# Kernel tuning notes

Hardware: AMD Instinct MI355X
Metric: run time of the kernel (lower is better)

The kernel has to match this reference:

```python
import jax, jax.numpy as jnp
import numpy as np

BN_EPS = 1e-5


def setup_inputs() -> dict:
    key = jax.random.key(0)
    ks = jax.random.split(key, 6)
    B, C, N = 8, 256, 4096
    C4 = C // 4
    return {
        "x": jax.random.normal(ks[0], (B, C, N), dtype=jnp.float32),
        "w_qk": jax.random.normal(ks[1], (C4, C), dtype=jnp.float32) * 0.05,  # shared q/k weight
        "w_v": jax.random.normal(ks[2], (C, C), dtype=jnp.float32) * 0.05,
        "b_v": jax.random.normal(ks[3], (C,), dtype=jnp.float32) * 0.05,
        "w_t": jax.random.normal(ks[4], (C, C), dtype=jnp.float32) * 0.05,
        "b_t": jax.random.normal(ks[5], (C,), dtype=jnp.float32) * 0.05,
        "gamma": jnp.ones((C,), dtype=jnp.float32),
        "beta": jnp.zeros((C,), dtype=jnp.float32),
        "run_mean": jnp.zeros((C,), dtype=jnp.float32),
        "run_var": jnp.ones((C,), dtype=jnp.float32),
    }


def reference(x, w_qk, w_v, b_v, w_t, b_t, gamma, beta, run_mean, run_var):
    # x: [B, C, N]; 1x1 Conv1d == channel matmul.
    x_q = jnp.einsum('oc,bcn->bno', w_qk, x)               # [B, N, C/4]
    x_k = jnp.einsum('oc,bcn->bon', w_qk, x)               # [B, C/4, N]
    energy = jnp.einsum('bno,bom->bnm', x_q, x_k)          # [B, N, N], NO 1/sqrt(d) scaling
    attn = jax.nn.softmax(energy, axis=-1)                 # softmax over last dim only
    x_v = jnp.einsum('oc,bcn->bon', w_v, x) + b_v[None, :, None]  # [B, C, N]
    x_r = jnp.einsum('bcn,bnm->bcm', x_v, attn)            # V @ attn (right-multiply, no transpose)
    t = jnp.einsum('oc,bcn->bon', w_t, x - x_r) + b_t[None, :, None]
    # BatchNorm1d (inference): per-channel affine with running stats
    inv = gamma / jnp.sqrt(run_var + BN_EPS)
    bn = t * inv[None, :, None] + (beta - run_mean * inv)[None, :, None]
    return x + jnp.maximum(bn, 0.0)
```

## Files before the change

### kernel.cpp

```cpp
#include <hip/hip_runtime.h>

#define Bb 8
#define Cc 256
#define C4 64
#define Nn 4096

typedef _Float16 half8 __attribute__((ext_vector_type(8)));
typedef float f32x4 __attribute__((ext_vector_type(4)));
typedef unsigned int u32;

__device__ __forceinline__ f32x4 fz4() {
  f32x4 z; z[0] = 0.f; z[1] = 0.f; z[2] = 0.f; z[3] = 0.f; return z;
}
__device__ __forceinline__ f32x4 mfma16(half8 a, half8 b, f32x4 c) {
  return __builtin_amdgcn_mfma_f32_16x16x32_f16(a, b, c, 0, 0, 0);
}
__device__ __forceinline__ u32 pkrtz(float a, float b) {
  typedef __fp16 h2n __attribute__((ext_vector_type(2)));
  h2n h = __builtin_amdgcn_cvt_pkrtz(a, b);
  return __builtin_bit_cast(u32, h);
}
__device__ __forceinline__ float ex2(float x) {
  float r;
  asm("v_exp_f32 %0, %1" : "=v"(r) : "v"(x));
  return r;
}
__device__ __forceinline__ void gll16(const void* g, void* l) {
  __builtin_amdgcn_global_load_lds(
      (const __attribute__((address_space(1))) u32*)g,
      (__attribute__((address_space(3))) u32*)l, 16, 0, 0);
}


__global__ void k0_weights(const float* __restrict__ wqk, const float* __restrict__ wv,
                           const float* __restrict__ wt,
                           _Float16* __restrict__ wqkh, _Float16* __restrict__ wqkl,
                           _Float16* __restrict__ wvf, _Float16* __restrict__ wtf) {
  int idx = blockIdx.x * 256 + threadIdx.x;
  if (idx < C4 * Cc) {
    int o = idx >> 8, c = idx & 255;
    float f = wqk[idx] * 1.2011224087864498f;
    _Float16 h = (_Float16)f;
    int off = ((((o >> 4) * 8 + (c >> 5)) * 4 + ((c >> 3) & 3)) * 16 + (o & 15)) * 8 + (c & 7);
    wqkh[off] = h;
    wqkl[off] = (_Float16)(f - (float)h);
  }
  if (idx < Cc * Cc) {
    int o = idx >> 8, k = idx & 255;
    int off = ((((o >> 4) * 8 + (k >> 5)) * 4 + ((k >> 3) & 3)) * 16 + (o & 15)) * 8 + (k & 7);
    wvf[off] = (_Float16)wv[idx];
    wtf[off] = (_Float16)wt[idx];
  }
}

__global__ __launch_bounds__(512) void k23_qkv(
    const float* __restrict__ x,
    const _Float16* __restrict__ wqkh, const _Float16* __restrict__ wqkl,
    const _Float16* __restrict__ wvf, const float* __restrict__ bv,
    _Float16* __restrict__ qkf, _Float16* __restrict__ xvf) {
  __shared__ _Float16 xh[64 * 264];
  const int bid = blockIdx.x;
  const int b = bid & 7, n0 = (bid >> 3) * 64, tid = threadIdx.x;
  {
    const int cc = tid >> 3, nn = (tid & 7) * 8;
    #pragma unroll
    for (int ph = 0; ph < 4; ++ph) {
      int c = cc + ph * 64;
      const float* src = x + ((size_t)(b * Cc + c)) * Nn + n0 + nn;
      float4 v0 = *(const float4*)(src);
      float4 v1 = *(const float4*)(src + 4);
      float vv[8] = {v0.x, v0.y, v0.z, v0.w, v1.x, v1.y, v1.z, v1.w};
      #pragma unroll
      for (int j = 0; j < 8; ++j) xh[(nn + j) * 264 + c] = (_Float16)vv[j];
    }
  }
  __syncthreads();
  const int w = tid >> 6, lane = tid & 63, l15 = lane & 15, l4 = lane >> 4;
  {
    const int fn = w >> 1, ob = (w & 1) * 32;
    f32x4 acc[2] = {fz4(), fz4()};
    #pragma unroll
    for (int kb = 0; kb < 8; ++kb) {
      half8 ah = *(const half8*)(xh + (fn * 16 + l15) * 264 + kb * 32 + l4 * 8);
      #pragma unroll
      for (int f = 0; f < 2; ++f) {
        const int ot = (ob >> 4) + f;
        half8 bh = *(const half8*)((const char*)wqkh + (ot * 8 + kb) * 1024 + lane * 16);
        half8 bl = *(const half8*)((const char*)wqkl + (ot * 8 + kb) * 1024 + lane * 16);
        acc[f] = mfma16(ah, bh, acc[f]);
        acc[f] = mfma16(ah, bl, acc[f]);
      }
    }
    #pragma unroll
    for (int f = 0; f < 2; ++f)
      #pragma unroll
      for (int i = 0; i < 4; ++i) {
        const int n = n0 + fn * 16 + l4 * 4 + i;
        const int o = ob + f * 16 + l15;
        int off = ((((b * 256 + (n >> 4)) * 2 + (o >> 5)) * 4 + ((o >> 3) & 3)) * 16 +
                   (n & 15)) * 8 + (o & 7);
        qkf[off] = (_Float16)acc[f][i];
      }
  }
  {
    const int cb = w * 32;
    f32x4 acc[2][4];
    #pragma unroll
    for (int a = 0; a < 2; ++a)
      #pragma unroll
      for (int q = 0; q < 4; ++q) acc[a][q] = fz4();
    #pragma unroll
    for (int kb = 0; kb < 8; ++kb) {
      half8 bfr[4];
      #pragma unroll
      for (int fnb = 0; fnb < 4; ++fnb)
        bfr[fnb] = *(const half8*)(xh + (fnb * 16 + l15) * 264 + kb * 32 + l4 * 8);
      #pragma unroll
      for (int fc = 0; fc < 2; ++fc) {
        const int ct = (cb >> 4) + fc;
        half8 a = *(const half8*)((const char*)wvf + (ct * 8 + kb) * 1024 + lane * 16);
        #pragma unroll
        for (int fnb = 0; fnb < 4; ++fnb)
          acc[fc][fnb] = mfma16(a, bfr[fnb], acc[fc][fnb]);
      }
    }
    #pragma unroll
    for (int fc = 0; fc < 2; ++fc)
      #pragma unroll
      for (int fnb = 0; fnb < 4; ++fnb)
        #pragma unroll
        for (int i = 0; i < 4; ++i) {
          const int c = cb + fc * 16 + l4 * 4 + i;
          const int n = n0 + fnb * 16 + l15;
          int off = ((((b * 16 + (c >> 4)) * 128 + (n >> 5)) * 4 + ((n >> 3) & 3)) * 16 +
                     (c & 15)) * 8 + (n & 7);
          xvf[off] = (_Float16)(acc[fc][fnb][i] + bv[c]);
        }
  }
}

__global__ __launch_bounds__(512, 4) void k4_stats(
    const _Float16* __restrict__ qkf, float* __restrict__ stats) {
  __shared__ float red[64][8];
  const int bid = blockIdx.x;
  const int b = bid & 7, n0 = (bid >> 3) * 64, tid = threadIdx.x;
  const int w = tid >> 6, lane = tid & 63, l15 = lane & 15, l4 = lane >> 4;
  const char* qbt = (const char*)qkf + (size_t)b * 524288;

  half8 qn_r[2][4];
  #pragma unroll
  for (int kb = 0; kb < 2; ++kb)
    #pragma unroll
    for (int fn = 0; fn < 4; ++fn)
      qn_r[kb][fn] = *(const half8*)(qbt + (((n0 >> 4) + fn) * 2 + kb) * 1024 + lane * 16);

  const char* qp = qbt + w * 2048 + lane * 16;
  half8 qa0 = *(const half8*)qp;
  half8 qa1 = *(const half8*)(qp + 1024);

  float sm[4] = {0.f, 0.f, 0.f, 0.f};
  for (int it = 0; it < 32; ++it) {
    f32x4 g[4] = {fz4(), fz4(), fz4(), fz4()};
    #pragma unroll
    for (int fn = 0; fn < 4; ++fn) g[fn] = mfma16(qa0, qn_r[0][fn], g[fn]);
    #pragma unroll
    for (int fn = 0; fn < 4; ++fn) g[fn] = mfma16(qa1, qn_r[1][fn], g[fn]);
    if (it < 31) qp += 16384;
    qa0 = *(const half8*)qp;
    qa1 = *(const half8*)(qp + 1024);
    #pragma unroll
    for (int fn = 0; fn < 4; ++fn)
      #pragma unroll
      for (int i = 0; i < 4; ++i)
        sm[fn] += ex2(g[fn][i] - 32.0f);
  }
  #pragma unroll
  for (int fn = 0; fn < 4; ++fn) {
    sm[fn] += __shfl_xor(sm[fn], 16, 64);
    sm[fn] += __shfl_xor(sm[fn], 32, 64);
  }
  if (l4 == 0) {
    #pragma unroll
    for (int fn = 0; fn < 4; ++fn) red[fn * 16 + l15][w] = sm[fn];
  }
  __syncthreads();
  if (tid < 64) {
    float t = 0.f;
    #pragma unroll
    for (int j = 0; j < 8; ++j) t += red[tid][j];
    stats[(size_t)b * Nn + n0 + tid] = 32.0f + log2f(t);
  }
}

__global__ __launch_bounds__(512, 2) void k5_main(
    const float* __restrict__ x,
    const _Float16* __restrict__ qkf, const _Float16* __restrict__ xvf,
    const float* __restrict__ stats,
    const _Float16* __restrict__ wtf, const float* __restrict__ bt,
    const float* __restrict__ gamma, const float* __restrict__ beta,
    const float* __restrict__ rmean, const float* __restrict__ rvar,
    float* __restrict__ out) {
  __shared__ __align__(16) char smem[122880];
  const int bid = blockIdx.x;
  const int b = bid & 7, m0 = (bid >> 3) * 128, tid = threadIdx.x;
  const int w = tid >> 6, lane = tid & 63, l15 = lane & 15, l4 = lane >> 4;
  const int wa = w >> 2;
  const int wb = w & 3;
  const size_t bq = (size_t)b * Nn;
  const char* qkt = (const char*)qkf + (size_t)b * 524288;
  const char* xvt = (const char*)xvf + (size_t)b * 2097152;
  const int key = l15 & 7;

  half8 qm_r[2][4];
  #pragma unroll
  for (int kb = 0; kb < 2; ++kb)
    #pragma unroll
    for (int fm = 0; fm < 4; ++fm)
      qm_r[kb][fm] = *(const half8*)(qkt + ((((m0 >> 4) + wa * 4 + fm) * 2) + kb) * 1024 +
                                     lane * 16);

  const char* qnsrc = qkt + 16384 + (size_t)tid * 16;
  const char* xvp = xvt + (size_t)w * 262144 + (size_t)lane * 16;
  const float* anp = stats + bq + wb * 16 + l4 * 4;

  f32x4 acc[4][4];
  #pragma unroll
  for (int a = 0; a < 4; ++a)
    #pragma unroll
    for (int q = 0; q < 4; ++q) acc[a][q] = fz4();

  gll16(qkt + (size_t)tid * 16, smem + w * 1024);
  gll16(qkt + 8192 + (size_t)tid * 16, smem + 8192 + w * 1024);
  #pragma unroll
  for (int j = 0; j < 4; ++j)
    gll16(xvp + (j >> 1) * 131072 + (j & 1) * 1024, smem + 57344 + (w * 4 + j) * 1024);
  float4 an = *(const float4*)anp;
  asm volatile("s_waitcnt vmcnt(0) lgkmcnt(0)" ::: "memory");
  __builtin_amdgcn_sched_barrier(0);
  __builtin_amdgcn_s_barrier();

  int br = 0, bw = 2;
  for (int it = 0; it < 64; ++it) {
    gll16(qnsrc, smem + bw * 8192 + w * 1024);
    if (it < 61) qnsrc += 8192;
    bw = bw == 2 ? 0 : bw + 1;
    const char* qb = smem + br * 8192;
    br = br == 2 ? 0 : br + 1;
    f32x4 g[4] = {fz4(), fz4(), fz4(), fz4()};
    #pragma unroll
    for (int kb = 0; kb < 2; ++kb) {
      half8 ah = *(const half8*)(qb + (wb * 2 + kb) * 1024 + lane * 16);
      #pragma unroll
      for (int fm = 0; fm < 4; ++fm)
        g[fm] = mfma16(ah, qm_r[kb][fm], g[fm]);
    }
    char* PTp = smem + 24576 + ((it & 1) << 14);
    #pragma unroll
    for (int fm = 0; fm < 4; ++fm) {
      uint2 pk;
      pk.x = pkrtz(ex2(g[fm][0] - an.x), ex2(g[fm][1] - an.y));
      pk.y = pkrtz(ex2(g[fm][2] - an.z), ex2(g[fm][3] - an.w));
      *(uint2*)(PTp + (wa * 64 + fm * 16 + l15) * 128 +
                ((wb * 32 + l4 * 8) ^ (key << 4))) = pk;
    }
    if (it < 63) anp += 64;
    an = *(const float4*)anp;
    asm volatile("s_waitcnt vmcnt(2) lgkmcnt(0)" ::: "memory");
    __builtin_amdgcn_sched_barrier(0);
    __builtin_amdgcn_s_barrier();
    const char* xvR = smem + 57344 + ((it & 1) << 15);
    __builtin_amdgcn_s_setprio(1);
    #pragma unroll
    for (int kb = 0; kb < 2; ++kb) {
      half8 pa[4], xb[4];
      #pragma unroll
      for (int fm = 0; fm < 4; ++fm)
        pa[fm] = *(const half8*)(PTp + (wa * 64 + fm * 16 + l15) * 128 +
                                 (((kb * 4 + l4) ^ key) * 16));
      #pragma unroll
      for (int fc = 0; fc < 4; ++fc)
        xb[fc] = *(const half8*)(xvR + ((wb * 4 + fc) * 2 + kb) * 1024 + lane * 16);
      #pragma unroll
      for (int fm = 0; fm < 4; ++fm)
        #pragma unroll
        for (int fc = 0; fc < 4; ++fc)
          acc[fm][fc] = mfma16(pa[fm], xb[fc], acc[fm][fc]);
    }
    __builtin_amdgcn_s_setprio(0);
    if (it < 63) xvp += 2048;
    char* xvD = smem + 57344 + (((it + 1) & 1) << 15) + (w * 4) * 1024;
    #pragma unroll
    for (int j = 0; j < 4; ++j)
      gll16(xvp + (j >> 1) * 131072 + (j & 1) * 1024, xvD + j * 1024);
  }
  asm volatile("s_waitcnt vmcnt(0) lgkmcnt(0)" ::: "memory");
  __builtin_amdgcn_sched_barrier(0);
  __builtin_amdgcn_s_barrier();

  _Float16* st = (_Float16*)smem;
  #pragma unroll
  for (int fm = 0; fm < 4; ++fm)
    #pragma unroll
    for (int fc = 0; fc < 4; ++fc) {
      int c = wb * 64 + fc * 16 + l15;
      int mb = wa * 64 + fm * 16 + l4 * 4;
      const float* xp = x + ((size_t)b * Cc + c) * Nn + m0 + mb;
      float4 v = *(const float4*)xp;
      float vv[4] = {v.x, v.y, v.z, v.w};
      #pragma unroll
      for (int i = 0; i < 4; ++i)
        st[(mb + i) * 264 + c] = (_Float16)(vv[i] - acc[fm][fc][i]);
    }
  __syncthreads();
  {
    const int ob = wb * 64, mh = wa * 64;
    f32x4 t[4][4];
    #pragma unroll
    for (int a = 0; a < 4; ++a)
      #pragma unroll
      for (int q = 0; q < 4; ++q) t[a][q] = fz4();
    #pragma unroll
    for (int kb = 0; kb < 8; ++kb) {
      half8 bfr[4];
      #pragma unroll
      for (int fm2 = 0; fm2 < 4; ++fm2)
        bfr[fm2] = *(const half8*)(st + (mh + fm2 * 16 + l15) * 264 + kb * 32 + l4 * 8);
      #pragma unroll
      for (int fo = 0; fo < 4; ++fo) {
        const int ot = (ob >> 4) + fo;
        half8 a = *(const half8*)((const char*)wtf + (ot * 8 + kb) * 1024 + lane * 16);
        #pragma unroll
        for (int fm2 = 0; fm2 < 4; ++fm2)
          t[fo][fm2] = mfma16(a, bfr[fm2], t[fo][fm2]);
      }
    }
    #pragma unroll
    for (int fo = 0; fo < 4; ++fo)
      #pragma unroll
      for (int i = 0; i < 4; ++i) {
        const int o = ob + fo * 16 + l4 * 4 + i;
        const float inv = gamma[o] * rsqrtf(rvar[o] + 1e-5f);
        const float addv = beta[o] - rmean[o] * inv;
        const float btv = bt[o];
        #pragma unroll
        for (int fm2 = 0; fm2 < 4; ++fm2) {
          const int m = m0 + mh + fm2 * 16 + l15;
          float tv = t[fo][fm2][i] + btv;
          float bn = tv * inv + addv;
          float xr = x[((size_t)b * Cc + o) * Nn + m];
          out[((size_t)b * Cc + o) * Nn + m] = xr + fmaxf(bn, 0.0f);
        }
      }
  }
}

extern "C" void kernel_launch(void* const* d_in, const int* in_sizes, int n_in,
                              void* d_out, int out_size, void* d_ws, size_t ws_size,
                              hipStream_t stream) {
  const float* x = (const float*)d_in[0];
  const float* wqk = (const float*)d_in[1];
  const float* wv = (const float*)d_in[2];
  const float* bv = (const float*)d_in[3];
  const float* wt = (const float*)d_in[4];
  const float* bt = (const float*)d_in[5];
  const float* gamma = (const float*)d_in[6];
  const float* beta = (const float*)d_in[7];
  const float* rmean = (const float*)d_in[8];
  const float* rvar = (const float*)d_in[9];
  float* out = (float*)d_out;

  char* ws = (char*)d_ws;
  size_t off = 0;
  auto alloc = [&](size_t nb) {
    char* p = ws + off;
    off += (nb + 255) & ~(size_t)255;
    return p;
  };
  _Float16* qkf = (_Float16*)alloc((size_t)Bb * Nn * C4 * 2);
  _Float16* xvf = (_Float16*)alloc((size_t)Bb * Cc * Nn * 2);
  float* stats = (float*)alloc((size_t)Bb * Nn * 4);
  _Float16* wqkh = (_Float16*)alloc((size_t)C4 * Cc * 2);
  _Float16* wqkl = (_Float16*)alloc((size_t)C4 * Cc * 2);
  _Float16* wvf = (_Float16*)alloc((size_t)Cc * Cc * 2);
  _Float16* wtf = (_Float16*)alloc((size_t)Cc * Cc * 2);

  k0_weights<<<dim3(256), dim3(256), 0, stream>>>(wqk, wv, wt, wqkh, wqkl, wvf, wtf);
  k23_qkv<<<dim3(512), dim3(512), 0, stream>>>(x, wqkh, wqkl, wvf, bv, qkf, xvf);
  k4_stats<<<dim3(512), dim3(512), 0, stream>>>(qkf, stats);
  k5_main<<<dim3(256), dim3(512), 0, stream>>>(x, qkf, xvf, stats, wtf, bt,
                                               gamma, beta, rmean, rvar, out);
}
```

Baseline: 149.2 us.

## Load Q/K and V tiles directly into registers instead of LDS staging

Drops the global_load_lds triple/double-buffered staging of the key tiles and V tiles in the main attention kernel. Each wave now prefetches its own fragments into ping-pong register sets one iteration ahead. The softmax row stats are preloaded once into LDS rather than fetched per iteration. LDS use falls from about 120 KB to 68 KB, which may allow two blocks per CU. The cost is duplicated global/L2 traffic across waves, higher register pressure, and a last-iteration prefetch that reads past the batch's slice.

```diff
diff --git a/kernel.cpp b/kernel.cpp
--- a/kernel.cpp
+++ b/kernel.cpp
@@ -24,11 +24,6 @@
   float r;
   asm("v_exp_f32 %0, %1" : "=v"(r) : "v"(x));
   return r;
-}
-__device__ __forceinline__ void gll16(const void* g, void* l) {
-  __builtin_amdgcn_global_load_lds(
-      (const __attribute__((address_space(1))) u32*)g,
-      (__attribute__((address_space(3))) u32*)l, 16, 0, 0);
 }
 
 
@@ -200,7 +195,7 @@
     const float* __restrict__ gamma, const float* __restrict__ beta,
     const float* __restrict__ rmean, const float* __restrict__ rvar,
     float* __restrict__ out) {
-  __shared__ __align__(16) char smem[122880];
+  __shared__ __align__(16) char smem[69632];
   const int bid = blockIdx.x;
   const int b = bid & 7, m0 = (bid >> 3) * 128, tid = threadIdx.x;
   const int w = tid >> 6, lane = tid & 63, l15 = lane & 15, l4 = lane >> 4;
@@ -210,6 +205,7 @@
   const char* qkt = (const char*)qkf + (size_t)b * 524288;
   const char* xvt = (const char*)xvf + (size_t)b * 2097152;
   const int key = l15 & 7;
+  float* anL = (float*)smem;
 
   half8 qm_r[2][4];
   #pragma unroll
@@ -219,9 +215,8 @@
       qm_r[kb][fm] = *(const half8*)(qkt + ((((m0 >> 4) + wa * 4 + fm) * 2) + kb) * 1024 +
                                      lane * 16);
 
-  const char* qnsrc = qkt + 16384 + (size_t)tid * 16;
-  const char* xvp = xvt + (size_t)w * 262144 + (size_t)lane * 16;
-  const float* anp = stats + bq + wb * 16 + l4 * 4;
+  const char* ah_base = qkt + (wb * 2) * 1024 + (size_t)lane * 16;
+  const char* xb_base = xvt + (size_t)(wb * 4) * 131072 + (size_t)lane * 16;
 
   f32x4 acc[4][4];
   #pragma unroll
@@ -229,71 +224,73 @@
     #pragma unroll
     for (int q = 0; q < 4; ++q) acc[a][q] = fz4();
 
-  gll16(qkt + (size_t)tid * 16, smem + w * 1024);
-  gll16(qkt + 8192 + (size_t)tid * 16, smem + 8192 + w * 1024);
-  #pragma unroll
-  for (int j = 0; j < 4; ++j)
-    gll16(xvp + (j >> 1) * 131072 + (j & 1) * 1024, smem + 57344 + (w * 4 + j) * 1024);
-  float4 an = *(const float4*)anp;
-  asm volatile("s_waitcnt vmcnt(0) lgkmcnt(0)" ::: "memory");
-  __builtin_amdgcn_sched_barrier(0);
-  __builtin_amdgcn_s_barrier();
-
-  int br = 0, bw = 2;
-  for (int it = 0; it < 64; ++it) {
-    gll16(qnsrc, smem + bw * 8192 + w * 1024);
-    if (it < 61) qnsrc += 8192;
-    bw = bw == 2 ? 0 : bw + 1;
-    const char* qb = smem + br * 8192;
-    br = br == 2 ? 0 : br + 1;
-    f32x4 g[4] = {fz4(), fz4(), fz4(), fz4()};
-    #pragma unroll
-    for (int kb = 0; kb < 2; ++kb) {
-      half8 ah = *(const half8*)(qb + (wb * 2 + kb) * 1024 + lane * 16);
-      #pragma unroll
-      for (int fm = 0; fm < 4; ++fm)
-        g[fm] = mfma16(ah, qm_r[kb][fm], g[fm]);
-    }
-    char* PTp = smem + 24576 + ((it & 1) << 14);
-    #pragma unroll
-    for (int fm = 0; fm < 4; ++fm) {
-      uint2 pk;
-      pk.x = pkrtz(ex2(g[fm][0] - an.x), ex2(g[fm][1] - an.y));
-      pk.y = pkrtz(ex2(g[fm][2] - an.z), ex2(g[fm][3] - an.w));
-      *(uint2*)(PTp + (wa * 64 + fm * 16 + l15) * 128 +
-                ((wb * 32 + l4 * 8) ^ (key << 4))) = pk;
-    }
-    if (it < 63) anp += 64;
-    an = *(const float4*)anp;
-    asm volatile("s_waitcnt vmcnt(2) lgkmcnt(0)" ::: "memory");
-    __builtin_amdgcn_sched_barrier(0);
-    __builtin_amdgcn_s_barrier();
-    const char* xvR = smem + 57344 + ((it & 1) << 15);
-    __builtin_amdgcn_s_setprio(1);
-    #pragma unroll
-    for (int kb = 0; kb < 2; ++kb) {
-      half8 pa[4], xb[4];
-      #pragma unroll
-      for (int fm = 0; fm < 4; ++fm)
-        pa[fm] = *(const half8*)(PTp + (wa * 64 + fm * 16 + l15) * 128 +
-                                 (((kb * 4 + l4) ^ key) * 16));
-      #pragma unroll
-      for (int fc = 0; fc < 4; ++fc)
-        xb[fc] = *(const half8*)(xvR + ((wb * 4 + fc) * 2 + kb) * 1024 + lane * 16);
-      #pragma unroll
-      for (int fm = 0; fm < 4; ++fm)
-        #pragma unroll
-        for (int fc = 0; fc < 4; ++fc)
-          acc[fm][fc] = mfma16(pa[fm], xb[fc], acc[fm][fc]);
-    }
-    __builtin_amdgcn_s_setprio(0);
-    if (it < 63) xvp += 2048;
-    char* xvD = smem + 57344 + (((it + 1) & 1) << 15) + (w * 4) * 1024;
-    #pragma unroll
-    for (int j = 0; j < 4; ++j)
-      gll16(xvp + (j >> 1) * 131072 + (j & 1) * 1024, xvD + j * 1024);
-  }
-  asm volatile("s_waitcnt vmcnt(0) lgkmcnt(0)" ::: "memory");
+  #pragma unroll
+  for (int j = 0; j < 2; ++j)
+    ((float4*)anL)[tid + 512 * j] = ((const float4*)(stats + bq))[tid + 512 * j];
+  half8 ahA[2], ahB[2], xbA[4][2], xbB[4][2];
+  #pragma unroll
+  for (int kb = 0; kb < 2; ++kb) ahA[kb] = *(const half8*)(ah_base + kb * 1024);
+  #pragma unroll
+  for (int fc = 0; fc < 4; ++fc)
+    #pragma unroll
+    for (int kb = 0; kb < 2; ++kb)
+      xbA[fc][kb] = *(const half8*)(xb_base + fc * 131072 + kb * 1024);
+  __syncthreads();
+
+#define K5_STEP(P, AH_CUR, AH_NXT, XB_CUR, XB_NXT)                                  \
+  {                                                                                \
+    const int it = it2 * 2 + (P);                                                  \
+                 \
+    {                                                                              \
+      const char* ahs = ah_base + (size_t)(it + 1) * 8192;                         \
+      _Pragma("unroll") for (int kb = 0; kb < 2; ++kb)                             \
+          AH_NXT[kb] = *(const half8*)(ahs + kb * 1024);                           \
+      const char* xbs = xb_base + (size_t)(it + 1) * 2048;                         \
+      _Pragma("unroll") for (int fc = 0; fc < 4; ++fc)                             \
+        _Pragma("unroll") for (int kb = 0; kb < 2; ++kb)                           \
+            XB_NXT[fc][kb] = *(const half8*)(xbs + fc * 131072 + kb * 1024);       \
+    }                                                                              \
+                                                               \
+    f32x4 g[4] = {fz4(), fz4(), fz4(), fz4()};                                     \
+    _Pragma("unroll") for (int kb = 0; kb < 2; ++kb)                               \
+      _Pragma("unroll") for (int fm = 0; fm < 4; ++fm)                             \
+          g[fm] = mfma16(AH_CUR[kb], qm_r[kb][fm], g[fm]);                         \
+                                  \
+    char* PTp = smem + 16384 + ((P) << 14);                                        \
+    {                                                                              \
+      float4 an = *(const float4*)(anL + it * 64 + wb * 16 + l4 * 4);              \
+      _Pragma("unroll") for (int fm = 0; fm < 4; ++fm) {                           \
+        uint2 pk;                                                                  \
+        pk.x = pkrtz(ex2(g[fm][0] - an.x), ex2(g[fm][1] - an.y));                  \
+        pk.y = pkrtz(ex2(g[fm][2] - an.z), ex2(g[fm][3] - an.w));                  \
+        *(uint2*)(PTp + (wa * 64 + fm * 16 + l15) * 128 +                          \
+                  ((wb * 32 + l4 * 8) ^ (key << 4))) = pk;                         \
+      }                                                                            \
+    }                                                                              \
+                                                     \
+    asm volatile("s_waitcnt lgkmcnt(0)" ::: "memory");                             \
+    __builtin_amdgcn_sched_barrier(0);                                             \
+    __builtin_amdgcn_s_barrier();                                                  \
+                                      \
+    __builtin_amdgcn_s_setprio(1);                                                 \
+    _Pragma("unroll") for (int kb = 0; kb < 2; ++kb) {                             \
+      half8 pa[4];                                                                 \
+      _Pragma("unroll") for (int fm = 0; fm < 4; ++fm)                             \
+          pa[fm] = *(const half8*)(PTp + (wa * 64 + fm * 16 + l15) * 128 +         \
+                                   (((kb * 4 + l4) ^ key) * 16));                  \
+      _Pragma("unroll") for (int fm = 0; fm < 4; ++fm)                             \
+        _Pragma("unroll") for (int fc = 0; fc < 4; ++fc)                           \
+            acc[fm][fc] = mfma16(pa[fm], XB_CUR[fc][kb], acc[fm][fc]);             \
+    }                                                                              \
+    __builtin_amdgcn_s_setprio(0);                                                 \
+  }
+
+  for (int it2 = 0; it2 < 32; ++it2) {
+    K5_STEP(0, ahA, ahB, xbA, xbB)
+    K5_STEP(1, ahB, ahA, xbB, xbA)
+  }
+#undef K5_STEP
+  asm volatile("s_waitcnt lgkmcnt(0)" ::: "memory");
   __builtin_amdgcn_sched_barrier(0);
   __builtin_amdgcn_s_barrier();
 
```

Result: faster. 140.2 us (-6.1%).
